# Kernel tuning notes

Hardware: AMD Instinct MI355X
Metric: run time of the kernel (lower is better)

## Reference

```python
import jax, jax.numpy as jnp
import numpy as np

N_NODES = 100000
N_EDGES = 1600000
EMBED = 64
HEADS = 8
HEAD_DIM = EMBED // HEADS
FFN = 4 * EMBED
EPS = 1e-5


def _layer_norm(x, g, b):
    m = jnp.mean(x, axis=-1, keepdims=True)
    v = jnp.mean(jnp.square(x - m), axis=-1, keepdims=True)
    return (x - m) * jax.lax.rsqrt(v + EPS) * g + b


def setup_inputs() -> dict:
    key = jax.random.key(0)
    ks = jax.random.split(key, 10)
    s = lambda fan_in: 1.0 / np.sqrt(fan_in)
    x = jax.random.normal(ks[0], (N_NODES, EMBED), dtype=jnp.float32)
    edge_indices = jax.random.randint(ks[1], (2, N_EDGES), 0, N_NODES, dtype=jnp.int64)
    attn_w = jax.random.uniform(ks[2], (EMBED, 3 * EMBED), jnp.float32, -s(EMBED), s(EMBED))
    attn_b = jnp.zeros((3 * EMBED,), jnp.float32)
    w1 = jax.random.uniform(ks[3], (EMBED, FFN), jnp.float32, -s(EMBED), s(EMBED))
    b1 = jnp.zeros((FFN,), jnp.float32)
    w2 = jax.random.uniform(ks[4], (FFN, EMBED), jnp.float32, -s(FFN), s(FFN))
    b2 = jnp.zeros((EMBED,), jnp.float32)
    ln1_g = jnp.ones((EMBED,), jnp.float32)
    ln1_b = jnp.zeros((EMBED,), jnp.float32)
    ln2_g = jnp.ones((EMBED,), jnp.float32)
    ln2_b = jnp.zeros((EMBED,), jnp.float32)
    return {"x": x, "edge_indices": edge_indices, "attn_w": attn_w, "attn_b": attn_b,
            "w1": w1, "b1": b1, "w2": w2, "b2": b2,
            "ln1_g": ln1_g, "ln1_b": ln1_b, "ln2_g": ln2_g, "ln2_b": ln2_b}


def _self_attention(x, edge_indices, attn_w, attn_b):
    n = x.shape[0]
    row, col = edge_indices[0], edge_indices[1]
    scale = EMBED ** (-0.5)  # note: original scales by embed_dim**-0.5
    qkv = (x @ attn_w + attn_b).reshape(n, HEADS, 3 * HEAD_DIM)
    q, k, v = jnp.split(qkv, 3, axis=2)  # each [N, H, Dh]
    alpha = jnp.sum(q[row] * k[col], axis=2) * scale  # [E, H]
    # sparse per-row softmax via segment reductions
    m = jax.ops.segment_max(alpha, row, num_segments=n)  # [N, H]
    e = jnp.exp(alpha - m[row])
    denom = jax.ops.segment_sum(e, row, num_segments=n)  # [N, H]
    weights = e / denom[row]  # [E, H]
    vals = v[col] * weights[:, :, None]  # [E, H, Dh]
    out = jax.ops.segment_sum(vals, row, num_segments=n)  # [N, H, Dh]
    return out.reshape(n, EMBED)


def reference(x, edge_indices, attn_w, attn_b, w1, b1, w2, b2, ln1_g, ln1_b, ln2_g, ln2_b):
    # post-norm (norm_first=False), dropout=0
    x = _layer_norm(x + _self_attention(x, edge_indices, attn_w, attn_b), ln1_g, ln1_b)
    ffn = jax.nn.relu(x @ w1 + b1) @ w2 + b2
    x = _layer_norm(x + ffn, ln2_g, ln2_b)
    return x
```

## Files before the change

### kernel.cpp

```cpp
#include <hip/hip_runtime.h>
#include <hip/hip_bf16.h>
#include <hip/hip_fp8.h>


#define WAVE 64
constexpr int BUCKET_SHIFT = 7;
constexpr int NBMAX = 800;

typedef __attribute__((ext_vector_type(8))) short bf16x8;
typedef __attribute__((ext_vector_type(4))) float f32x4;
typedef __attribute__((ext_vector_type(2))) float f32x2;

__device__ __forceinline__ float bfbits_lo(unsigned u) {
  return __uint_as_float(u << 16);
}
__device__ __forceinline__ float bfbits_hi(unsigned u) {
  return __uint_as_float(u & 0xffff0000u);
}
__device__ __forceinline__ unsigned f2bf_pk(float a, float b) {
  unsigned ua = __float_as_uint(a);
  unsigned ub = __float_as_uint(b);
  ua = (ua + 0x7fff + ((ua >> 16) & 1)) >> 16;
  ub = (ub + 0x7fff + ((ub >> 16) & 1)) & 0xffff0000u;
  return ua | ub;
}
__device__ __forceinline__ unsigned short f2bf1(float a) {
  unsigned ua = __float_as_uint(a);
  ua = (ua + 0x7fff + ((ua >> 16) & 1)) >> 16;
  return (unsigned short)ua;
}

#if defined(__has_builtin)
#if __has_builtin(__builtin_amdgcn_cvt_pk_f32_fp8) && \
    __has_builtin(__builtin_amdgcn_cvt_pk_fp8_f32)
#define FP8_HW 1
#endif
#endif

#ifdef FP8_HW
#define FP8PK0(w) __builtin_amdgcn_cvt_pk_f32_fp8((int)(w), false)
#define FP8PK1(w) __builtin_amdgcn_cvt_pk_f32_fp8((int)(w), true)
__device__ __forceinline__ unsigned fp8enc4(float a, float b, float c,
                                            float d) {
  int r = __builtin_amdgcn_cvt_pk_fp8_f32(a, b, 0, false);
  r = __builtin_amdgcn_cvt_pk_fp8_f32(c, d, r, true);
  return (unsigned)r;
}
#else
__device__ __forceinline__ f32x2 fp8pk_sw(unsigned w, int sh) {
  __hip_fp8_e4m3 a, b;
  a.__x = (unsigned char)((w >> sh) & 0xff);
  b.__x = (unsigned char)((w >> (sh + 8)) & 0xff);
  f32x2 r;
  r.x = (float)a;
  r.y = (float)b;
  return r;
}
#define FP8PK0(w) fp8pk_sw((w), 0)
#define FP8PK1(w) fp8pk_sw((w), 16)
__device__ __forceinline__ unsigned fp8enc4(float a, float b, float c,
                                            float d) {
  __hip_fp8_e4m3 qa(a), qb(b), qc(c), qd(d);
  return (unsigned)qa.__x | ((unsigned)qb.__x << 8) |
         ((unsigned)qc.__x << 16) | ((unsigned)qd.__x << 24);
}
#endif

__device__ __forceinline__ float dot8_fp8(uint2 w, const float qv[8]) {
  f32x2 a = FP8PK0(w.x), b = FP8PK1(w.x), c = FP8PK0(w.y), d = FP8PK1(w.y);
  return a.x * qv[0] + a.y * qv[1] + b.x * qv[2] + b.y * qv[3] + c.x * qv[4] +
         c.y * qv[5] + d.x * qv[6] + d.y * qv[7];
}
__device__ __forceinline__ void acc8_fp8(uint2 w, float ee, float acc[8]) {
  f32x2 a = FP8PK0(w.x), b = FP8PK1(w.x), c = FP8PK0(w.y), d = FP8PK1(w.y);
  acc[0] += ee * a.x;
  acc[1] += ee * a.y;
  acc[2] += ee * b.x;
  acc[3] += ee * b.y;
  acc[4] += ee * c.x;
  acc[5] += ee * c.y;
  acc[6] += ee * d.x;
  acc[7] += ee * d.y;
}

__global__ __launch_bounds__(256) void cvt_w2(
    const float* __restrict__ aw, const float* __restrict__ w1,
    const float* __restrict__ w2, unsigned short* __restrict__ awT,
    unsigned short* __restrict__ w1T, unsigned short* __restrict__ w2T) {
  int tid = blockIdx.x * 256 + threadIdx.x;
  int stride = gridDim.x * 256;
  for (int i = tid; i < 192 * 64; i += stride) {
    int nn = i >> 6, kk = i & 63;
    awT[i] = f2bf1(aw[kk * 192 + nn]);
  }
  for (int i = tid; i < 256 * 64; i += stride) {
    int nn = i >> 6, kk = i & 63;
    w1T[i] = f2bf1(w1[kk * 256 + nn]);
  }
  for (int i = tid; i < 64 * 256; i += stride) {
    int nn = i >> 8, kk = i & 255;
    w2T[i] = f2bf1(w2[kk * 64 + nn]);
  }
}

__global__ __launch_bounds__(256) void cvt_x(const float* __restrict__ x,
                                             unsigned short* __restrict__ xb,
                                             int total8) {
  int i = blockIdx.x * 256 + threadIdx.x;
  int stride = gridDim.x * 256;
  const float4* xf = (const float4*)x;
  uint4* xo = (uint4*)xb;
  for (; i < total8; i += stride) {
    float4 a = xf[2 * i], b = xf[2 * i + 1];
    uint4 st = make_uint4(f2bf_pk(a.x, a.y), f2bf_pk(a.z, a.w),
                          f2bf_pk(b.x, b.y), f2bf_pk(b.z, b.w));
    xo[i] = st;
  }
}

template <int NCOLS, int K, int MODE>
__global__ __launch_bounds__(256) void mfma_gemm(
    const unsigned short* __restrict__ A, const unsigned short* __restrict__ BT,
    const float* __restrict__ bias, unsigned short* __restrict__ out_q,
    unsigned char* __restrict__ out_kv8, unsigned short* __restrict__ out_h,
    const unsigned short* __restrict__ resid, const float* __restrict__ g,
    const float* __restrict__ beta, float* __restrict__ out_f, int n) {
  constexpr int KP = K + 8;
  constexpr int NT = NCOLS / 16;
  constexpr int NKC = K / 32;
  __shared__ unsigned short sB[NCOLS * KP];

  const int tid = threadIdx.x;
  {
    const uint4* src = (const uint4*)BT;
    for (int idx = tid; idx < NCOLS * K / 8; idx += 256) {
      int nn = idx / (K / 8), kq = idx % (K / 8);
      *(uint4*)&sB[nn * KP + kq * 8] = src[idx];
    }
  }
  __syncthreads();

  const int wid = tid >> 6, lane = tid & 63;
  const int l15 = lane & 15, quad = lane >> 4;
  const int rowbase = blockIdx.x * 128 + wid * 32;

  bf16x8 afrag[2][NKC];
#pragma unroll
  for (int rg = 0; rg < 2; rg++) {
    int row = rowbase + rg * 16 + l15;
    if (row >= n) row = n - 1;
    const bf16x8* ap = (const bf16x8*)(A + (size_t)row * K);
#pragma unroll
    for (int kc = 0; kc < NKC; kc++) afrag[rg][kc] = ap[kc * 4 + quad];
  }

  f32x4 acc[2][NT];
#pragma unroll
  for (int rg = 0; rg < 2; rg++)
#pragma unroll
    for (int t = 0; t < NT; t++) acc[rg][t] = (f32x4){0.f, 0.f, 0.f, 0.f};

#pragma unroll
  for (int t = 0; t < NT; t++) {
#pragma unroll
    for (int kc = 0; kc < NKC; kc++) {
      bf16x8 b = *(const bf16x8*)&sB[(t * 16 + l15) * KP + kc * 32 + quad * 8];
      acc[0][t] = __builtin_amdgcn_mfma_f32_16x16x32_bf16(b, afrag[0][kc],
                                                          acc[0][t], 0, 0, 0);
      acc[1][t] = __builtin_amdgcn_mfma_f32_16x16x32_bf16(b, afrag[1][kc],
                                                          acc[1][t], 0, 0, 0);
    }
  }

  if (MODE == 0) {
#pragma unroll
    for (int rg = 0; rg < 2; rg++) {
      int row = rowbase + rg * 16 + l15;
      if (row >= n) continue;
#pragma unroll
      for (int t = 0; t < NT; t++) {
        int c0 = t * 16 + quad * 4;
        float4 bb = *(const float4*)&bias[c0];
        float v0 = acc[rg][t].x + bb.x, v1 = acc[rg][t].y + bb.y;
        float v2 = acc[rg][t].z + bb.z, v3 = acc[rg][t].w + bb.w;
        int hh = c0 / 24, rem = c0 % 24;
        if (rem < 8) {
          v0 *= 0.125f;
          v1 *= 0.125f;
          v2 *= 0.125f;
          v3 *= 0.125f;
          *(uint2*)(out_q + (size_t)row * 64 + hh * 8 + rem) =
              make_uint2(f2bf_pk(v0, v1), f2bf_pk(v2, v3));
        } else if (rem < 16) {
          *(unsigned*)(out_kv8 + (size_t)row * 128 + hh * 8 + (rem - 8)) =
              fp8enc4(v0, v1, v2, v3);
        } else {
          *(unsigned*)(out_kv8 + (size_t)row * 128 + 64 + hh * 8 + (rem - 16)) =
              fp8enc4(v0, v1, v2, v3);
        }
      }
    }
  } else if (MODE == 1) {
#pragma unroll
    for (int rg = 0; rg < 2; rg++) {
      int row = rowbase + rg * 16 + l15;
      if (row >= n) continue;
#pragma unroll
      for (int t = 0; t < NT; t++) {
        int c0 = t * 16 + quad * 4;
        float4 bb = *(const float4*)&bias[c0];
        float v0 = fmaxf(acc[rg][t].x + bb.x, 0.f);
        float v1 = fmaxf(acc[rg][t].y + bb.y, 0.f);
        float v2 = fmaxf(acc[rg][t].z + bb.z, 0.f);
        float v3 = fmaxf(acc[rg][t].w + bb.w, 0.f);
        *(uint2*)(out_h + (size_t)row * NCOLS + c0) =
            make_uint2(f2bf_pk(v0, v1), f2bf_pk(v2, v3));
      }
    }
  } else {
#pragma unroll
    for (int rg = 0; rg < 2; rg++) {
      int row = rowbase + rg * 16 + l15;
      bool ok = row < n;
      int rowc = ok ? row : n - 1;
      float vals[4][4];
      float ps = 0.f, pq = 0.f;
#pragma unroll
      for (int t = 0; t < 4; t++) {
        int c0 = t * 16 + quad * 4;
        float4 bb = *(const float4*)&bias[c0];
        uint2 rr = *(const uint2*)&resid[(size_t)rowc * 64 + c0];
        vals[t][0] = acc[rg][t].x + bb.x + bfbits_lo(rr.x);
        vals[t][1] = acc[rg][t].y + bb.y + bfbits_hi(rr.x);
        vals[t][2] = acc[rg][t].z + bb.z + bfbits_lo(rr.y);
        vals[t][3] = acc[rg][t].w + bb.w + bfbits_hi(rr.y);
#pragma unroll
        for (int r = 0; r < 4; r++) {
          ps += vals[t][r];
          pq += vals[t][r] * vals[t][r];
        }
      }
      ps += __shfl_xor(ps, 16);
      ps += __shfl_xor(ps, 32);
      pq += __shfl_xor(pq, 16);
      pq += __shfl_xor(pq, 32);
      float mean = ps * (1.f / 64.f);
      float var = pq * (1.f / 64.f) - mean * mean;
      float inv = rsqrtf(var + 1e-5f);
      if (ok) {
#pragma unroll
        for (int t = 0; t < 4; t++) {
          int c0 = t * 16 + quad * 4;
          float4 gg = *(const float4*)&g[c0];
          float4 be = *(const float4*)&beta[c0];
          float4 o = make_float4((vals[t][0] - mean) * inv * gg.x + be.x,
                                 (vals[t][1] - mean) * inv * gg.y + be.y,
                                 (vals[t][2] - mean) * inv * gg.z + be.z,
                                 (vals[t][3] - mean) * inv * gg.w + be.w);
          *(float4*)&out_f[(size_t)row * 64 + c0] = o;
        }
      }
    }
  }
}

__global__ void detect_kernel(const int* __restrict__ e, unsigned* flag) {
  unsigned v = 0;
  for (int i = threadIdx.x; i < 2048; i += 256) v |= (unsigned)e[2 * i + 1];
#pragma unroll
  for (int m = 1; m < WAVE; m <<= 1) v |= (unsigned)__shfl_xor((int)v, m);
  if ((threadIdx.x & 63) == 0 && v) atomicOr(flag, 1u);
}

__device__ __forceinline__ int edge_row(const int* e, int i, bool is64) {
  return is64 ? e[2 * (size_t)i] : e[i];
}
__device__ __forceinline__ int edge_col(const int* e, int i, int E, bool is64) {
  return is64 ? e[2 * ((size_t)E + i)] : e[(size_t)E + i];
}

__global__ __launch_bounds__(256) void partition_count(
    const int* __restrict__ e, int E, const unsigned* __restrict__ flag,
    int* __restrict__ G, int NB, int CH) {
  __shared__ int h[NBMAX];
  bool is64 = (*flag == 0u);
  for (int b = threadIdx.x; b < NB; b += 256) h[b] = 0;
  __syncthreads();
  int c0 = blockIdx.x * CH, c1 = min(E, c0 + CH);
  for (int i = c0 + threadIdx.x; i < c1; i += 256)
    atomicAdd(&h[edge_row(e, i, is64) >> BUCKET_SHIFT], 1);
  __syncthreads();
  for (int b = threadIdx.x; b < NB; b += 256) G[b * 256 + blockIdx.x] = h[b];
}

__global__ __launch_bounds__(1024) void scan_reduce(const int* __restrict__ in,
                                                    int n,
                                                    int* __restrict__ bsum) {
  __shared__ int sdata[16];
  int tid = threadIdx.x;
  int idx = blockIdx.x * 1024 + tid;
  int v = (idx < n) ? in[idx] : 0;
#pragma unroll
  for (int m = 1; m < WAVE; m <<= 1) v += __shfl_xor(v, m);
  if ((tid & 63) == 0) sdata[tid >> 6] = v;
  __syncthreads();
  if (tid < 16) {
    int s = sdata[tid];
#pragma unroll
    for (int m = 1; m < 16; m <<= 1) s += __shfl_xor(s, m);
    if (tid == 0) bsum[blockIdx.x] = s;
  }
}

__global__ __launch_bounds__(256) void scan_top(const int* __restrict__ bsum,
                                                int nb, int* __restrict__ bpre) {
  __shared__ int wsum[4];
  int tid = threadIdx.x;
  int lane = tid & 63, wid = tid >> 6;
  int v = (tid < nb) ? bsum[tid] : 0;
  int incl = v;
#pragma unroll
  for (int m = 1; m < WAVE; m <<= 1) {
    int t = __shfl_up(incl, m);
    if (lane >= m) incl += t;
  }
  if (lane == 63) wsum[wid] = incl;
  __syncthreads();
  int add = 0;
  for (int w = 0; w < wid; w++) add += wsum[w];
  if (tid < nb) bpre[tid] = add + incl - v;
}

__global__ __launch_bounds__(1024) void scan_apply(
    const int* __restrict__ in, int n, const int* __restrict__ bpre,
    int* __restrict__ outscan) {
  __shared__ int wtot[16];
  __shared__ int wexcl[16];
  int tid = threadIdx.x;
  int idx = blockIdx.x * 1024 + tid;
  int v = (idx < n) ? in[idx] : 0;
  int incl = v;
#pragma unroll
  for (int m = 1; m < WAVE; m <<= 1) {
    int t = __shfl_up(incl, m);
    if ((tid & 63) >= m) incl += t;
  }
  int wid = tid >> 6;
  if ((tid & 63) == 63) wtot[wid] = incl;
  __syncthreads();
  if (tid < 16) {
    int w = wtot[tid];
    int wi = w;
#pragma unroll
    for (int m = 1; m < 16; m <<= 1) {
      int t = __shfl_up(wi, m);
      if (tid >= m) wi += t;
    }
    wexcl[tid] = wi - w;
  }
  __syncthreads();
  if (idx < n) outscan[idx] = bpre[blockIdx.x] + wexcl[wid] + incl - v;
}

__global__ __launch_bounds__(256) void partition_scatter(
    const int* __restrict__ e, int E, const unsigned* __restrict__ flag,
    const int* __restrict__ scanG, unsigned* __restrict__ ebuf, int NB,
    int CH) {
  __shared__ int base[NBMAX];
  bool is64 = (*flag == 0u);
  for (int b = threadIdx.x; b < NB; b += 256)
    base[b] = scanG[b * 256 + blockIdx.x];
  __syncthreads();
  int c0 = blockIdx.x * CH, c1 = min(E, c0 + CH);
  for (int i = c0 + threadIdx.x; i < c1; i += 256) {
    int r = edge_row(e, i, is64);
    int c = edge_col(e, i, E, is64);
    int pos = atomicAdd(&base[r >> BUCKET_SHIFT], 1);
    ebuf[pos] = ((unsigned)(r & 127) << 17) | (unsigned)c;
  }
}

__global__ __launch_bounds__(256) void bucket_csr(
    const unsigned* __restrict__ ebuf, const int* __restrict__ scanG,
    int* __restrict__ ecol, int* __restrict__ rowstart, int n, int NB, int E) {
  __shared__ int cnt[128], offs[128], cur[128];
  const int b = blockIdx.x;
  const int tid = threadIdx.x;
  const int start = scanG[b * 256];
  const int end = (b + 1 < NB) ? scanG[(b + 1) * 256] : E;
  if (tid < 128) cnt[tid] = 0;
  __syncthreads();
  for (int i = start + tid; i < end; i += 256)
    atomicAdd(&cnt[(ebuf[i] >> 17) & 127], 1);
  __syncthreads();
  if (tid < 128) offs[tid] = cnt[tid];
  __syncthreads();
  for (int s = 1; s < 128; s <<= 1) {
    int t = 0;
    if (tid < 128 && tid >= s) t = offs[tid - s];
    __syncthreads();
    if (tid < 128) offs[tid] += t;
    __syncthreads();
  }
  if (tid < 128) {
    int excl = offs[tid] - cnt[tid];
    cur[tid] = start + excl;
    int gr = (b << BUCKET_SHIFT) + tid;
    if (gr < n) rowstart[gr] = start + excl;
  }
  if (b == NB - 1 && tid == 0) rowstart[n] = E;
  __syncthreads();
  for (int i = start + tid; i < end; i += 256) {
    unsigned p = ebuf[i];
    int pos = atomicAdd(&cur[(p >> 17) & 127], 1);
    ecol[pos] = (int)(p & 0x1FFFF);
  }
}

__global__ __launch_bounds__(256) void attn_ln_kernel(
    const unsigned short* __restrict__ xb,
    const unsigned short* __restrict__ qbuf,
    const unsigned char* __restrict__ kv8, const int* __restrict__ rowstart,
    const int* __restrict__ ecol, const float* __restrict__ g,
    const float* __restrict__ beta, unsigned short* __restrict__ x1b, int n) {
  int wave = threadIdx.x >> 6;
  int lane = threadIdx.x & 63;
  int node = blockIdx.x * 4 + wave;
  if (node >= n) return;
  const int e = lane >> 3, h = lane & 7;

  uint4 qp = ((const uint4*)(qbuf + (size_t)node * 64))[h];
  float qv[8] = {bfbits_lo(qp.x), bfbits_hi(qp.x), bfbits_lo(qp.y),
                 bfbits_hi(qp.y), bfbits_lo(qp.z), bfbits_hi(qp.z),
                 bfbits_lo(qp.w), bfbits_hi(qp.w)};

  int start = rowstart[node];
  int cnt = rowstart[node + 1] - start;
  float den = 0.f;
  float acc[8] = {0.f, 0.f, 0.f, 0.f, 0.f, 0.f, 0.f, 0.f};

  int iters = (cnt + 7) >> 3;
  int it = 0;
  for (; it + 2 <= iters; it += 2) {
    int i0 = it * 8 + e;
    int i1 = i0 + 8;
    bool v1 = i1 < cnt;
    int c0 = ecol[start + i0];
    int c1 = ecol[start + (v1 ? i1 : i0)];
    const unsigned char* r0 = kv8 + (size_t)c0 * 128 + h * 8;
    const unsigned char* r1 = kv8 + (size_t)c1 * 128 + h * 8;
    uint2 kw0 = *(const uint2*)r0;
    uint2 vw0 = *(const uint2*)(r0 + 64);
    uint2 kw1 = *(const uint2*)r1;
    uint2 vw1 = *(const uint2*)(r1 + 64);
    float a0 = dot8_fp8(kw0, qv);
    float a1 = dot8_fp8(kw1, qv);
    float e0 = __expf(a0);
    float e1 = v1 ? __expf(a1) : 0.f;
    den += e0 + e1;
    acc8_fp8(vw0, e0, acc);
    acc8_fp8(vw1, e1, acc);
  }
  if (it < iters) {
    int i0 = it * 8 + e;
    bool v0 = i0 < cnt;
    int c0 = ecol[start + (v0 ? i0 : 0)];
    const unsigned char* r0 = kv8 + (size_t)c0 * 128 + h * 8;
    uint2 kw0 = *(const uint2*)r0;
    uint2 vw0 = *(const uint2*)(r0 + 64);
    float a0 = dot8_fp8(kw0, qv);
    float e0 = v0 ? __expf(a0) : 0.f;
    den += e0;
    acc8_fp8(vw0, e0, acc);
  }

#pragma unroll
  for (int m = 8; m < 64; m <<= 1) {
    den += __shfl_xor(den, m);
#pragma unroll
    for (int j = 0; j < 8; j++) acc[j] += __shfl_xor(acc[j], m);
  }

  float invden = (cnt > 0) ? 1.f / den : 0.f;

  uint4 xr = *(const uint4*)(xb + (size_t)node * 64 + h * 8);
  float v[8];
  v[0] = bfbits_lo(xr.x) + acc[0] * invden;
  v[1] = bfbits_hi(xr.x) + acc[1] * invden;
  v[2] = bfbits_lo(xr.y) + acc[2] * invden;
  v[3] = bfbits_hi(xr.y) + acc[3] * invden;
  v[4] = bfbits_lo(xr.z) + acc[4] * invden;
  v[5] = bfbits_hi(xr.z) + acc[5] * invden;
  v[6] = bfbits_lo(xr.w) + acc[6] * invden;
  v[7] = bfbits_hi(xr.w) + acc[7] * invden;

  float ps = 0.f;
#pragma unroll
  for (int j = 0; j < 8; j++) ps += v[j];
#pragma unroll
  for (int m = 1; m < 8; m <<= 1) ps += __shfl_xor(ps, m);
  float mean = ps * (1.f / 64.f);
  float pq = 0.f;
#pragma unroll
  for (int j = 0; j < 8; j++) {
    float d = v[j] - mean;
    pq += d * d;
  }
#pragma unroll
  for (int m = 1; m < 8; m <<= 1) pq += __shfl_xor(pq, m);
  float inv = rsqrtf(pq * (1.f / 64.f) + 1e-5f);

  if (e == 0) {
    const float4* gr = (const float4*)(g + h * 8);
    const float4* br = (const float4*)(beta + h * 8);
    float4 ga = gr[0], gb = gr[1];
    float4 ba = br[0], bb = br[1];
    float o[8];
    o[0] = (v[0] - mean) * inv * ga.x + ba.x;
    o[1] = (v[1] - mean) * inv * ga.y + ba.y;
    o[2] = (v[2] - mean) * inv * ga.z + ba.z;
    o[3] = (v[3] - mean) * inv * ga.w + ba.w;
    o[4] = (v[4] - mean) * inv * gb.x + bb.x;
    o[5] = (v[5] - mean) * inv * gb.y + bb.y;
    o[6] = (v[6] - mean) * inv * gb.z + bb.z;
    o[7] = (v[7] - mean) * inv * gb.w + bb.w;
    *(uint4*)(x1b + (size_t)node * 64 + h * 8) =
        make_uint4(f2bf_pk(o[0], o[1]), f2bf_pk(o[2], o[3]),
                   f2bf_pk(o[4], o[5]), f2bf_pk(o[6], o[7]));
  }
}

extern "C" void kernel_launch(void* const* d_in, const int* in_sizes, int n_in,
                              void* d_out, int out_size, void* d_ws,
                              size_t ws_size, hipStream_t stream) {
  const float* x = (const float*)d_in[0];
  const int* edges = (const int*)d_in[1];
  const float* attn_w = (const float*)d_in[2];
  const float* attn_b = (const float*)d_in[3];
  const float* w1 = (const float*)d_in[4];
  const float* b1 = (const float*)d_in[5];
  const float* w2 = (const float*)d_in[6];
  const float* b2 = (const float*)d_in[7];
  const float* g1 = (const float*)d_in[8];
  const float* bb1 = (const float*)d_in[9];
  const float* g2 = (const float*)d_in[10];
  const float* bb2 = (const float*)d_in[11];

  const int N = in_sizes[0] / 64;
  const int E = in_sizes[1] / 2;
  const int NB = (N + 127) >> BUCKET_SHIFT;
  const int CH = (E + 255) / 256;
  const int NG = NB * 256;

  char* ws = (char*)d_ws;
  size_t oq = 0;
  size_t okv = oq + (size_t)N * 128;
  size_t ox1b = okv + (size_t)N * 128;
  size_t oxb = ox1b + (size_t)N * 128;
  size_t oh = oxb + (size_t)N * 128;
  size_t oawT = oh + (size_t)N * 512;
  size_t ow1T = oawT + 192 * 64 * 2;
  size_t ow2T = ow1T + 256 * 64 * 2;
  size_t oG = ow2T + 64 * 256 * 2;
  size_t oscanG = oG + (size_t)NG * 4;
  size_t oebuf = oscanG + (size_t)NG * 4;
  size_t oecol = oebuf + (size_t)E * 4;
  size_t orowstart = oecol + (size_t)E * 4;
  size_t obsum = orowstart + (size_t)(N + 4) * 4;
  size_t obpre = obsum + 1024;
  size_t oflag = obpre + 1024;

  unsigned short* qbuf = (unsigned short*)(ws + oq);
  unsigned char* kv8 = (unsigned char*)(ws + okv);
  unsigned short* x1b = (unsigned short*)(ws + ox1b);
  unsigned short* xb = (unsigned short*)(ws + oxb);
  unsigned short* hbuf = (unsigned short*)(ws + oh);
  unsigned short* awT = (unsigned short*)(ws + oawT);
  unsigned short* w1T = (unsigned short*)(ws + ow1T);
  unsigned short* w2T = (unsigned short*)(ws + ow2T);
  int* G = (int*)(ws + oG);
  int* scanG = (int*)(ws + oscanG);
  unsigned* ebuf = (unsigned*)(ws + oebuf);
  int* ecol = (int*)(ws + oecol);
  int* rowstart = (int*)(ws + orowstart);
  int* bsum = (int*)(ws + obsum);
  int* bpre = (int*)(ws + obpre);
  unsigned* flag = (unsigned*)(ws + oflag);

  hipMemsetAsync(flag, 0, 4, stream);

  cvt_w2<<<32, 256, 0, stream>>>(attn_w, w1, w2, awT, w1T, w2T);
  cvt_x<<<512, 256, 0, stream>>>(x, xb, N * 8);

  detect_kernel<<<1, 256, 0, stream>>>(edges, flag);
  partition_count<<<256, 256, 0, stream>>>(edges, E, flag, G, NB, CH);
  int nscan = (NG + 1023) / 1024;
  scan_reduce<<<nscan, 1024, 0, stream>>>(G, NG, bsum);
  scan_top<<<1, 256, 0, stream>>>(bsum, nscan, bpre);
  scan_apply<<<nscan, 1024, 0, stream>>>(G, NG, bpre, scanG);
  partition_scatter<<<256, 256, 0, stream>>>(edges, E, flag, scanG, ebuf, NB,
                                             CH);
  bucket_csr<<<NB, 256, 0, stream>>>(ebuf, scanG, ecol, rowstart, N, NB, E);

  const int gblocks = (N + 127) / 128;

  mfma_gemm<192, 64, 0><<<gblocks, 256, 0, stream>>>(
      xb, awT, attn_b, qbuf, kv8, nullptr, nullptr, nullptr, nullptr, nullptr,
      N);

  attn_ln_kernel<<<(N + 3) / 4, 256, 0, stream>>>(xb, qbuf, kv8, rowstart,
                                                  ecol, g1, bb1, x1b, N);

  mfma_gemm<256, 64, 1><<<gblocks, 256, 0, stream>>>(
      x1b, w1T, b1, nullptr, nullptr, hbuf, nullptr, nullptr, nullptr, nullptr,
      N);

  mfma_gemm<64, 256, 2><<<gblocks, 256, 0, stream>>>(
      hbuf, w2T, b2, nullptr, nullptr, nullptr, x1b, g2, bb2, (float*)d_out,
      N);
}
```

Baseline: 284.0 us.

## Store K/V in fp16 with fdot2 and packed-half accumulation; fuse x conversion into QKV GEMM

Replaces the fp8 K/V cache with fp16 (doubling gather bytes per edge) and keeps Q in fp16, so the attention kernel can use fdot2 for scores and packed half FMAs for value accumulation instead of unpacking fp8 to fp32. It removes the separate x-to-bf16 conversion kernel by converting fp32 x inside the QKV GEMM's A-fragment load, and has the attention residual read fp32 x directly. The trade is more gather bandwidth and fp16 accumulation precision in exchange for fewer conversion instructions and one less launch.

```diff
diff --git a/kernel.cpp b/kernel.cpp
--- a/kernel.cpp
+++ b/kernel.cpp
@@ -1,6 +1,5 @@
 #include <hip/hip_runtime.h>
 #include <hip/hip_bf16.h>
-#include <hip/hip_fp8.h>
 
 
 #define WAVE 64
@@ -10,6 +9,7 @@
 typedef __attribute__((ext_vector_type(8))) short bf16x8;
 typedef __attribute__((ext_vector_type(4))) float f32x4;
 typedef __attribute__((ext_vector_type(2))) float f32x2;
+typedef __attribute__((ext_vector_type(2))) _Float16 h16x2;
 
 __device__ __forceinline__ float bfbits_lo(unsigned u) {
   return __uint_as_float(u << 16);
@@ -31,56 +31,56 @@
 }
 
 #if defined(__has_builtin)
-#if __has_builtin(__builtin_amdgcn_cvt_pk_f32_fp8) && \
-    __has_builtin(__builtin_amdgcn_cvt_pk_fp8_f32)
-#define FP8_HW 1
+#if __has_builtin(__builtin_amdgcn_cvt_pkrtz)
+#define HAS_PKRTZ 1
+#endif
+#if __has_builtin(__builtin_amdgcn_fdot2)
+#define HAS_FDOT2 1
 #endif
 #endif
 
-#ifdef FP8_HW
-#define FP8PK0(w) __builtin_amdgcn_cvt_pk_f32_fp8((int)(w), false)
-#define FP8PK1(w) __builtin_amdgcn_cvt_pk_f32_fp8((int)(w), true)
-__device__ __forceinline__ unsigned fp8enc4(float a, float b, float c,
-                                            float d) {
-  int r = __builtin_amdgcn_cvt_pk_fp8_f32(a, b, 0, false);
-  r = __builtin_amdgcn_cvt_pk_fp8_f32(c, d, r, true);
-  return (unsigned)r;
-}
+__device__ __forceinline__ unsigned f2h_pk(float a, float b) {
+#ifdef HAS_PKRTZ
+  auto h = __builtin_amdgcn_cvt_pkrtz(a, b);
+  return __builtin_bit_cast(unsigned, h);
 #else
-__device__ __forceinline__ f32x2 fp8pk_sw(unsigned w, int sh) {
-  __hip_fp8_e4m3 a, b;
-  a.__x = (unsigned char)((w >> sh) & 0xff);
-  b.__x = (unsigned char)((w >> (sh + 8)) & 0xff);
-  f32x2 r;
-  r.x = (float)a;
-  r.y = (float)b;
-  return r;
-}
-#define FP8PK0(w) fp8pk_sw((w), 0)
-#define FP8PK1(w) fp8pk_sw((w), 16)
-__device__ __forceinline__ unsigned fp8enc4(float a, float b, float c,
-                                            float d) {
-  __hip_fp8_e4m3 qa(a), qb(b), qc(c), qd(d);
-  return (unsigned)qa.__x | ((unsigned)qb.__x << 8) |
-         ((unsigned)qc.__x << 16) | ((unsigned)qd.__x << 24);
-}
+  h16x2 h;
+  h.x = (_Float16)a;
+  h.y = (_Float16)b;
+  return __builtin_bit_cast(unsigned, h);
 #endif
-
-__device__ __forceinline__ float dot8_fp8(uint2 w, const float qv[8]) {
-  f32x2 a = FP8PK0(w.x), b = FP8PK1(w.x), c = FP8PK0(w.y), d = FP8PK1(w.y);
-  return a.x * qv[0] + a.y * qv[1] + b.x * qv[2] + b.y * qv[3] + c.x * qv[4] +
-         c.y * qv[5] + d.x * qv[6] + d.y * qv[7];
-}
-__device__ __forceinline__ void acc8_fp8(uint2 w, float ee, float acc[8]) {
-  f32x2 a = FP8PK0(w.x), b = FP8PK1(w.x), c = FP8PK0(w.y), d = FP8PK1(w.y);
-  acc[0] += ee * a.x;
-  acc[1] += ee * a.y;
-  acc[2] += ee * b.x;
-  acc[3] += ee * b.y;
-  acc[4] += ee * c.x;
-  acc[5] += ee * c.y;
-  acc[6] += ee * d.x;
-  acc[7] += ee * d.y;
+}
+
+__device__ __forceinline__ float dot8_f16(uint4 kw, uint4 qw) {
+#ifdef HAS_FDOT2
+  float s = __builtin_amdgcn_fdot2(__builtin_bit_cast(h16x2, kw.x),
+                                   __builtin_bit_cast(h16x2, qw.x), 0.f, false);
+  s = __builtin_amdgcn_fdot2(__builtin_bit_cast(h16x2, kw.y),
+                             __builtin_bit_cast(h16x2, qw.y), s, false);
+  s = __builtin_amdgcn_fdot2(__builtin_bit_cast(h16x2, kw.z),
+                             __builtin_bit_cast(h16x2, qw.z), s, false);
+  s = __builtin_amdgcn_fdot2(__builtin_bit_cast(h16x2, kw.w),
+                             __builtin_bit_cast(h16x2, qw.w), s, false);
+  return s;
+#else
+  unsigned kk[4] = {kw.x, kw.y, kw.z, kw.w};
+  unsigned qq[4] = {qw.x, qw.y, qw.z, qw.w};
+  float s = 0.f;
+#pragma unroll
+  for (int i = 0; i < 4; i++) {
+    h16x2 a = __builtin_bit_cast(h16x2, kk[i]);
+    h16x2 b = __builtin_bit_cast(h16x2, qq[i]);
+    s += (float)a.x * (float)b.x + (float)a.y * (float)b.y;
+  }
+  return s;
+#endif
+}
+
+__device__ __forceinline__ void acc8_f16_pk(uint4 w, h16x2 e2, h16x2 acc[4]) {
+  acc[0] = __builtin_elementwise_fma(__builtin_bit_cast(h16x2, w.x), e2, acc[0]);
+  acc[1] = __builtin_elementwise_fma(__builtin_bit_cast(h16x2, w.y), e2, acc[1]);
+  acc[2] = __builtin_elementwise_fma(__builtin_bit_cast(h16x2, w.z), e2, acc[2]);
+  acc[3] = __builtin_elementwise_fma(__builtin_bit_cast(h16x2, w.w), e2, acc[3]);
 }
 
 __global__ __launch_bounds__(256) void cvt_w2(
@@ -103,26 +103,12 @@
   }
 }
 
-__global__ __launch_bounds__(256) void cvt_x(const float* __restrict__ x,
-                                             unsigned short* __restrict__ xb,
-                                             int total8) {
-  int i = blockIdx.x * 256 + threadIdx.x;
-  int stride = gridDim.x * 256;
-  const float4* xf = (const float4*)x;
-  uint4* xo = (uint4*)xb;
-  for (; i < total8; i += stride) {
-    float4 a = xf[2 * i], b = xf[2 * i + 1];
-    uint4 st = make_uint4(f2bf_pk(a.x, a.y), f2bf_pk(a.z, a.w),
-                          f2bf_pk(b.x, b.y), f2bf_pk(b.z, b.w));
-    xo[i] = st;
-  }
-}
-
 template <int NCOLS, int K, int MODE>
 __global__ __launch_bounds__(256) void mfma_gemm(
-    const unsigned short* __restrict__ A, const unsigned short* __restrict__ BT,
-    const float* __restrict__ bias, unsigned short* __restrict__ out_q,
-    unsigned char* __restrict__ out_kv8, unsigned short* __restrict__ out_h,
+    const unsigned short* __restrict__ A, const float* __restrict__ Af,
+    const unsigned short* __restrict__ BT, const float* __restrict__ bias,
+    unsigned short* __restrict__ out_q, unsigned char* __restrict__ out_kv,
+    unsigned short* __restrict__ out_h,
     const unsigned short* __restrict__ resid, const float* __restrict__ g,
     const float* __restrict__ beta, float* __restrict__ out_f, int n) {
   constexpr int KP = K + 8;
@@ -149,9 +135,26 @@
   for (int rg = 0; rg < 2; rg++) {
     int row = rowbase + rg * 16 + l15;
     if (row >= n) row = n - 1;
-    const bf16x8* ap = (const bf16x8*)(A + (size_t)row * K);
-#pragma unroll
-    for (int kc = 0; kc < NKC; kc++) afrag[rg][kc] = ap[kc * 4 + quad];
+    if constexpr (MODE == 0) {
+      const float4* ap = (const float4*)(Af + (size_t)row * K);
+#pragma unroll
+      for (int kc = 0; kc < NKC; kc++) {
+        float4 a = ap[kc * 8 + quad * 2], b = ap[kc * 8 + quad * 2 + 1];
+        union {
+          unsigned u[4];
+          bf16x8 v;
+        } z;
+        z.u[0] = f2bf_pk(a.x, a.y);
+        z.u[1] = f2bf_pk(a.z, a.w);
+        z.u[2] = f2bf_pk(b.x, b.y);
+        z.u[3] = f2bf_pk(b.z, b.w);
+        afrag[rg][kc] = z.v;
+      }
+    } else {
+      const bf16x8* ap = (const bf16x8*)(A + (size_t)row * K);
+#pragma unroll
+      for (int kc = 0; kc < NKC; kc++) afrag[rg][kc] = ap[kc * 4 + quad];
+    }
   }
 
   f32x4 acc[2][NT];
@@ -190,13 +193,14 @@
           v2 *= 0.125f;
           v3 *= 0.125f;
           *(uint2*)(out_q + (size_t)row * 64 + hh * 8 + rem) =
-              make_uint2(f2bf_pk(v0, v1), f2bf_pk(v2, v3));
+              make_uint2(f2h_pk(v0, v1), f2h_pk(v2, v3));
         } else if (rem < 16) {
-          *(unsigned*)(out_kv8 + (size_t)row * 128 + hh * 8 + (rem - 8)) =
-              fp8enc4(v0, v1, v2, v3);
+          *(uint2*)(out_kv + ((size_t)row << 8) + hh * 16 + (rem - 8) * 2) =
+              make_uint2(f2h_pk(v0, v1), f2h_pk(v2, v3));
         } else {
-          *(unsigned*)(out_kv8 + (size_t)row * 128 + 64 + hh * 8 + (rem - 16)) =
-              fp8enc4(v0, v1, v2, v3);
+          *(uint2*)(out_kv + ((size_t)row << 8) + 128 + hh * 16 +
+                    (rem - 16) * 2) =
+              make_uint2(f2h_pk(v0, v1), f2h_pk(v2, v3));
         }
       }
     }
@@ -313,7 +317,8 @@
 }
 
 __global__ __launch_bounds__(256) void scan_top(const int* __restrict__ bsum,
-                                                int nb, int* __restrict__ bpre) {
+                                                int nb,
+                                                int* __restrict__ bpre) {
   __shared__ int wsum[4];
   int tid = threadIdx.x;
   int lane = tid & 63, wid = tid >> 6;
@@ -418,9 +423,8 @@
 }
 
 __global__ __launch_bounds__(256) void attn_ln_kernel(
-    const unsigned short* __restrict__ xb,
-    const unsigned short* __restrict__ qbuf,
-    const unsigned char* __restrict__ kv8, const int* __restrict__ rowstart,
+    const float* __restrict__ x, const unsigned short* __restrict__ qbuf,
+    const unsigned char* __restrict__ kv, const int* __restrict__ rowstart,
     const int* __restrict__ ecol, const float* __restrict__ g,
     const float* __restrict__ beta, unsigned short* __restrict__ x1b, int n) {
   int wave = threadIdx.x >> 6;
@@ -429,15 +433,17 @@
   if (node >= n) return;
   const int e = lane >> 3, h = lane & 7;
 
-  uint4 qp = ((const uint4*)(qbuf + (size_t)node * 64))[h];
-  float qv[8] = {bfbits_lo(qp.x), bfbits_hi(qp.x), bfbits_lo(qp.y),
-                 bfbits_hi(qp.y), bfbits_lo(qp.z), bfbits_hi(qp.z),
-                 bfbits_lo(qp.w), bfbits_hi(qp.w)};
+  uint4 qp = ((const uint4*)qbuf)[(size_t)node * 8 + h];
 
   int start = rowstart[node];
   int cnt = rowstart[node + 1] - start;
+  const int* ec = ecol + start;
+  const int koff = h * 16, voff = 128 + h * 16;
+
   float den = 0.f;
-  float acc[8] = {0.f, 0.f, 0.f, 0.f, 0.f, 0.f, 0.f, 0.f};
+  h16x2 acch[4];
+#pragma unroll
+  for (int j = 0; j < 4; j++) acch[j] = (h16x2){(_Float16)0.f, (_Float16)0.f};
 
   int iters = (cnt + 7) >> 3;
   int it = 0;
@@ -445,54 +451,66 @@
     int i0 = it * 8 + e;
     int i1 = i0 + 8;
     bool v1 = i1 < cnt;
-    int c0 = ecol[start + i0];
-    int c1 = ecol[start + (v1 ? i1 : i0)];
-    const unsigned char* r0 = kv8 + (size_t)c0 * 128 + h * 8;
-    const unsigned char* r1 = kv8 + (size_t)c1 * 128 + h * 8;
-    uint2 kw0 = *(const uint2*)r0;
-    uint2 vw0 = *(const uint2*)(r0 + 64);
-    uint2 kw1 = *(const uint2*)r1;
-    uint2 vw1 = *(const uint2*)(r1 + 64);
-    float a0 = dot8_fp8(kw0, qv);
-    float a1 = dot8_fp8(kw1, qv);
+    int c0 = ec[i0];
+    int c1 = ec[v1 ? i1 : i0];
+    const unsigned char* r0 = kv + ((size_t)c0 << 8);
+    const unsigned char* r1 = kv + ((size_t)c1 << 8);
+    uint4 kw0 = *(const uint4*)(r0 + koff);
+    uint4 vw0 = *(const uint4*)(r0 + voff);
+    uint4 kw1 = *(const uint4*)(r1 + koff);
+    uint4 vw1 = *(const uint4*)(r1 + voff);
+    float a0 = dot8_f16(kw0, qp);
+    float a1 = dot8_f16(kw1, qp);
     float e0 = __expf(a0);
     float e1 = v1 ? __expf(a1) : 0.f;
     den += e0 + e1;
-    acc8_fp8(vw0, e0, acc);
-    acc8_fp8(vw1, e1, acc);
+    h16x2 ep0 = __builtin_bit_cast(h16x2, f2h_pk(e0, e0));
+    h16x2 ep1 = __builtin_bit_cast(h16x2, f2h_pk(e1, e1));
+    acc8_f16_pk(vw0, ep0, acch);
+    acc8_f16_pk(vw1, ep1, acch);
   }
   if (it < iters) {
     int i0 = it * 8 + e;
     bool v0 = i0 < cnt;
-    int c0 = ecol[start + (v0 ? i0 : 0)];
-    const unsigned char* r0 = kv8 + (size_t)c0 * 128 + h * 8;
-    uint2 kw0 = *(const uint2*)r0;
-    uint2 vw0 = *(const uint2*)(r0 + 64);
-    float a0 = dot8_fp8(kw0, qv);
+    int c0 = ec[v0 ? i0 : 0];
+    const unsigned char* r0 = kv + ((size_t)c0 << 8);
+    uint4 kw0 = *(const uint4*)(r0 + koff);
+    uint4 vw0 = *(const uint4*)(r0 + voff);
+    float a0 = dot8_f16(kw0, qp);
     float e0 = v0 ? __expf(a0) : 0.f;
     den += e0;
-    acc8_fp8(vw0, e0, acc);
+    h16x2 ep0 = __builtin_bit_cast(h16x2, f2h_pk(e0, e0));
+    acc8_f16_pk(vw0, ep0, acch);
   }
 
 #pragma unroll
   for (int m = 8; m < 64; m <<= 1) {
     den += __shfl_xor(den, m);
 #pragma unroll
-    for (int j = 0; j < 8; j++) acc[j] += __shfl_xor(acc[j], m);
-  }
+    for (int j = 0; j < 4; j++) {
+      unsigned o = __shfl_xor(__builtin_bit_cast(unsigned, acch[j]), m);
+      acch[j] += __builtin_bit_cast(h16x2, o);
+    }
+  }
+
+  float acc[8] = {(float)acch[0].x, (float)acch[0].y, (float)acch[1].x,
+                  (float)acch[1].y, (float)acch[2].x, (float)acch[2].y,
+                  (float)acch[3].x, (float)acch[3].y};
 
   float invden = (cnt > 0) ? 1.f / den : 0.f;
 
-  uint4 xr = *(const uint4*)(xb + (size_t)node * 64 + h * 8);
+  const float* xr = x + (size_t)node * 64 + h * 8;
+  float4 x0 = *(const float4*)xr;
+  float4 x1 = *(const float4*)(xr + 4);
   float v[8];
-  v[0] = bfbits_lo(xr.x) + acc[0] * invden;
-  v[1] = bfbits_hi(xr.x) + acc[1] * invden;
-  v[2] = bfbits_lo(xr.y) + acc[2] * invden;
-  v[3] = bfbits_hi(xr.y) + acc[3] * invden;
-  v[4] = bfbits_lo(xr.z) + acc[4] * invden;
-  v[5] = bfbits_hi(xr.z) + acc[5] * invden;
-  v[6] = bfbits_lo(xr.w) + acc[6] * invden;
-  v[7] = bfbits_hi(xr.w) + acc[7] * invden;
+  v[0] = x0.x + acc[0] * invden;
+  v[1] = x0.y + acc[1] * invden;
+  v[2] = x0.z + acc[2] * invden;
+  v[3] = x0.w + acc[3] * invden;
+  v[4] = x1.x + acc[4] * invden;
+  v[5] = x1.y + acc[5] * invden;
+  v[6] = x1.z + acc[6] * invden;
+  v[7] = x1.w + acc[7] * invden;
 
   float ps = 0.f;
 #pragma unroll
@@ -555,9 +573,8 @@
   char* ws = (char*)d_ws;
   size_t oq = 0;
   size_t okv = oq + (size_t)N * 128;
-  size_t ox1b = okv + (size_t)N * 128;
-  size_t oxb = ox1b + (size_t)N * 128;
-  size_t oh = oxb + (size_t)N * 128;
+  size_t ox1b = okv + (size_t)N * 256;
+  size_t oh = ox1b + (size_t)N * 128;
   size_t oawT = oh + (size_t)N * 512;
   size_t ow1T = oawT + 192 * 64 * 2;
   size_t ow2T = ow1T + 256 * 64 * 2;
@@ -571,9 +588,8 @@
   size_t oflag = obpre + 1024;
 
   unsigned short* qbuf = (unsigned short*)(ws + oq);
-  unsigned char* kv8 = (unsigned char*)(ws + okv);
+  unsigned char* kvb = (unsigned char*)(ws + okv);
   unsigned short* x1b = (unsigned short*)(ws + ox1b);
-  unsigned short* xb = (unsigned short*)(ws + oxb);
   unsigned short* hbuf = (unsigned short*)(ws + oh);
   unsigned short* awT = (unsigned short*)(ws + oawT);
   unsigned short* w1T = (unsigned short*)(ws + ow1T);
@@ -587,10 +603,9 @@
   int* bpre = (int*)(ws + obpre);
   unsigned* flag = (unsigned*)(ws + oflag);
 
-  hipMemsetAsync(flag, 0, 4, stream);
+  (void)hipMemsetAsync(flag, 0, 4, stream);
 
   cvt_w2<<<32, 256, 0, stream>>>(attn_w, w1, w2, awT, w1T, w2T);
-  cvt_x<<<512, 256, 0, stream>>>(x, xb, N * 8);
 
   detect_kernel<<<1, 256, 0, stream>>>(edges, flag);
   partition_count<<<256, 256, 0, stream>>>(edges, E, flag, G, NB, CH);
@@ -605,17 +620,17 @@
   const int gblocks = (N + 127) / 128;
 
   mfma_gemm<192, 64, 0><<<gblocks, 256, 0, stream>>>(
-      xb, awT, attn_b, qbuf, kv8, nullptr, nullptr, nullptr, nullptr, nullptr,
-      N);
-
-  attn_ln_kernel<<<(N + 3) / 4, 256, 0, stream>>>(xb, qbuf, kv8, rowstart,
-                                                  ecol, g1, bb1, x1b, N);
+      nullptr, x, awT, attn_b, qbuf, kvb, nullptr, nullptr, nullptr, nullptr,
+      nullptr, N);
+
+  attn_ln_kernel<<<(N + 3) / 4, 256, 0, stream>>>(x, qbuf, kvb, rowstart, ecol,
+                                                  g1, bb1, x1b, N);
 
   mfma_gemm<256, 64, 1><<<gblocks, 256, 0, stream>>>(
-      x1b, w1T, b1, nullptr, nullptr, hbuf, nullptr, nullptr, nullptr, nullptr,
-      N);
+      x1b, nullptr, w1T, b1, nullptr, nullptr, hbuf, nullptr, nullptr, nullptr,
+      nullptr, N);
 
   mfma_gemm<64, 256, 2><<<gblocks, 256, 0, stream>>>(
-      hbuf, w2T, b2, nullptr, nullptr, nullptr, x1b, g2, bb2, (float*)d_out,
-      N);
-}
+      hbuf, nullptr, w2T, b2, nullptr, nullptr, nullptr, x1b, g2, bb2,
+      (float*)d_out, N);
+}
```

Measured after the change: 288.6 us. No clear change (+1.6%).
